# Optimization experiments

Hardware: AMD Instinct MI355X
Metric: run time of the kernel (lower is better)

Reference implementation:

```python
import jax, jax.numpy as jnp
import numpy as np
from jax import lax

N = 4096  # minibatch size / number of points


def _pairwise_dist(x):
    # x: (N, d) -> (N, N) euclidean distance matrix, symmetric, zero diagonal
    sq = jnp.sum(x * x, axis=-1)
    d2 = sq[:, None] + sq[None, :] - 2.0 * (x @ x.T)
    d2 = jnp.maximum(d2, 0.0)
    d = jnp.sqrt(d2)
    return d * (1.0 - jnp.eye(x.shape[0], dtype=x.dtype))


def setup_inputs() -> dict:
    key = jax.random.key(0)
    k1, k2 = jax.random.split(key)
    x_in = jax.random.normal(k1, (N, 32), dtype=jnp.float32)   # input-space points
    x_lat = jax.random.normal(k2, (N, 8), dtype=jnp.float32)   # latent-space points
    return {
        "input_distances": _pairwise_dist(x_in),
        "latent_distances": _pairwise_dist(x_lat),
    }


def _mst_edges(D):
    """Prim's algorithm on a dense distance matrix.

    Returns (N-1, 2) int32 edges (parent_in_tree, new_node). With distinct
    edge weights (random point clouds) the MST is unique, so this matches
    the original union-find/Kruskal get_mst_edges(one_root=True) edge set.
    """
    n = D.shape[0]
    in_tree0 = jnp.zeros((n,), dtype=bool).at[0].set(True)
    dist0 = D[0]                          # best distance from tree to each node
    parent0 = jnp.zeros((n,), dtype=jnp.int32)

    def step(carry, _):
        dist, parent, in_tree = carry
        masked = jnp.where(in_tree, jnp.inf, dist)
        j = jnp.argmin(masked).astype(jnp.int32)  # nearest non-tree node
        edge = jnp.stack([parent[j], j])
        in_tree = in_tree.at[j].set(True)
        row = D[j]                         # relax: distances via new node j
        better = row < dist
        dist = jnp.where(better, row, dist)
        parent = jnp.where(better, j, parent)
        return (dist, parent, in_tree), edge

    _, edges = lax.scan(step, (dist0, parent0, in_tree0), None, length=n - 1)
    return edges  # (N-1, 2)


def _select(D, pairs):
    return D[pairs[:, 0], pairs[:, 1]]


def reference(input_distances, latent_distances):
    pairs1 = _mst_edges(input_distances)
    pairs2 = _mst_edges(latent_distances)
    sig1 = _select(input_distances, pairs1)
    sig2 = _select(latent_distances, pairs2)
    sig1_2 = _select(latent_distances, pairs1)
    sig2_1 = _select(input_distances, pairs2)
    distance1_2 = jnp.sum((sig1 - sig1_2) ** 2)
    distance2_1 = jnp.sum((sig2 - sig2_1) ** 2)
    return distance1_2 + distance2_1
```

## Files before the change

### kernel.cpp

```cpp
#include <hip/hip_runtime.h>
#include <stdint.h>


#define NPTS 4096
#define NCHUNK 64
#define NBLK 1024
#define ROUNDS 12

typedef unsigned long long u64;

__device__ __forceinline__ u64 umin64(u64 a, u64 b) { return a < b ? a : b; }

__device__ __forceinline__ u64 pack_edge(float w, int i, int j) {
    unsigned wb = __float_as_uint(w);
    int u = i < j ? i : j;
    int v = i < j ? j : i;
    return ((u64)wb << 24) | ((u64)(unsigned)u << 12) | (u64)(unsigned)v;
}

__device__ __forceinline__ u64 wave_min64(u64 v) {
    #pragma unroll
    for (int off = 32; off; off >>= 1)
        v = umin64(v, __shfl_down(v, (unsigned)off, 64));
    return v;
}

__global__ __launch_bounds__(256) void tile_k(
    const float* __restrict__ D1, const float* __restrict__ D2,
    u64* __restrict__ cand) {
    int pb = blockIdx.x >> 12;
    int t  = blockIdx.x & 4095;
    int r = t >> 6, c = t & 63;
    if (r > c) return;
    const float* __restrict__ D = pb ? D2 : D1;
    u64* __restrict__ cnd = cand + (size_t)pb * NPTS * NCHUNK;

    __shared__ float ts[64][65];
    int R0 = r << 6, C0 = c << 6;
    int tid = threadIdx.x;

    #pragma unroll
    for (int e = 0; e < 4; ++e) {
        int idx4 = tid + e * 256;
        int row = idx4 >> 4, c4 = idx4 & 15;
        const float4* __restrict__ rp =
            (const float4*)(D + (size_t)(R0 + row) * NPTS + C0);
        float4 w = rp[c4];
        ts[row][c4 * 4    ] = w.x; ts[row][c4 * 4 + 1] = w.y;
        ts[row][c4 * 4 + 2] = w.z; ts[row][c4 * 4 + 3] = w.w;
    }
    __syncthreads();

    int wave = tid >> 6, lane = tid & 63;
    if (wave == 0) {
        int i = R0 + lane;
        float wm = 3.4e38f; int jm = 0;
        if (r == c) {
            for (int j = 0; j < 64; ++j) {
                float x = ts[lane][j];
                if ((C0 + j) != i && x < wm) { wm = x; jm = C0 + j; }
            }
        } else {
            for (int j = 0; j < 64; ++j) {
                float x = ts[lane][j];
                if (x < wm) { wm = x; jm = C0 + j; }
            }
        }
        cnd[i * NCHUNK + c] = pack_edge(wm, i, jm);
    } else if (wave == 1 && r != c) {
        int jcol = C0 + lane;
        float wm = 3.4e38f; int im = 0;
        for (int k2 = 0; k2 < 64; ++k2) {
            float x = ts[k2][lane];
            if (x < wm) { wm = x; im = R0 + k2; }
        }
        cnd[jcol * NCHUNK + r] = pack_edge(wm, jcol, im);
    }
}

__global__ __launch_bounds__(256) void finalize_k(
    u64* __restrict__ best, const u64* __restrict__ cand,
    int* __restrict__ done, float* __restrict__ out) {
    if (blockIdx.x == 0 && threadIdx.x == 0) {
        done[0] = 0; done[1] = 0; out[0] = 0.f;
    }
    int pb = blockIdx.x >> 10;
    int rb = blockIdx.x & (NBLK - 1);
    const u64* __restrict__ cnd = cand + (size_t)pb * NPTS * NCHUNK;
    int wave = threadIdx.x >> 6, lane = threadIdx.x & 63;
    int i = rb * 4 + wave;
    u64 bv = wave_min64(cnd[i * NCHUNK + lane]);
    if (lane == 0) best[pb * NPTS + i] = bv;
}

__global__ __launch_bounds__(256) void warm_k(
    const float* __restrict__ D1, const float* __restrict__ D2,
    u64* __restrict__ best, const int* __restrict__ comp,
    const int* __restrict__ done, u64* __restrict__ cand) {
    int pb = blockIdx.x >> 10;
    if (done[pb]) return;
    int rb = blockIdx.x & (NBLK - 1);
    const float* __restrict__ D = pb ? D2 : D1;
    const int* __restrict__ cmpg = comp + pb * NPTS;
    u64* __restrict__ bst = best + pb * NPTS;
    u64* __restrict__ cnd = cand + (size_t)pb * NPTS * NCHUNK;

    int wave = threadIdx.x >> 6, lane = threadIdx.x & 63;
    int i = rb * 4 + wave;
    int ci = cmpg[i];

    u64 live = ~0ull;
    bool dead = false;
    u64 c = cnd[i * NCHUNK + lane];
    if (c != ~0ull) {
        int u = (int)((c >> 12) & 0xFFF), v = (int)(c & 0xFFF);
        int j = (u == i) ? v : u;
        if (cmpg[j] != ci) live = c;
        else dead = true;
    }

    u64 extra = ~0ull;
    u64 mask = __ballot(dead);
    if (mask) {
        const float4* __restrict__ rowf = (const float4*)(D + (size_t)i * NPTS);
        const int4* __restrict__ cmp4 = (const int4*)cmpg;
        int g = lane >> 4, m16 = lane & 15;
        while (mask) {
            int kq = -1;
            #pragma unroll
            for (int s = 0; s < 4; ++s) {
                int kk = mask ? (int)(__ffsll((long long)mask) - 1) : -1;
                if (kk >= 0) mask &= mask - 1;
                if (s == g) kq = kk;
            }
            u64 e = ~0ull;
            if (kq >= 0) {
                float4 w = rowf[kq * 16 + m16];
                int4 cj = cmp4[kq * 16 + m16];
                int j0 = kq * 64 + m16 * 4;
                if (cj.x != ci) e = umin64(e, pack_edge(w.x, i, j0));
                if (cj.y != ci) e = umin64(e, pack_edge(w.y, i, j0 + 1));
                if (cj.z != ci) e = umin64(e, pack_edge(w.z, i, j0 + 2));
                if (cj.w != ci) e = umin64(e, pack_edge(w.w, i, j0 + 3));
            }
            #pragma unroll
            for (int off = 8; off; off >>= 1)
                e = umin64(e, __shfl_down(e, (unsigned)off, 16));
            if (kq >= 0 && m16 == 0) {
                cnd[i * NCHUNK + kq] = e;
                extra = umin64(extra, e);
            }
        }
    }
    u64 rmin = wave_min64(umin64(live, extra));
    if (lane == 0 && rmin != ~0ull && rmin < bst[ci]) atomicMin(&bst[ci], rmin);
}

__global__ __launch_bounds__(1024) void contract_k(
    const float* __restrict__ D1, const float* __restrict__ D2,
    u64* __restrict__ best, int* __restrict__ comp,
    int* __restrict__ done, float* __restrict__ out, int identity) {
    int pb = blockIdx.x;
    if (!identity && done[pb]) return;
    u64* __restrict__ bst = best + pb * NPTS;
    int* __restrict__ cmp = comp + pb * NPTS;

    __shared__ int link_s[NPTS];
    __shared__ float red_s[16];
    __shared__ int flag_s;
    int t = threadIdx.x;
    float loss = 0.f;

    int eu[4], ev[4], nl[4];
    bool act[4];

    for (int q = 0; q < 4; ++q) {
        int c = t + q * 1024;
        u64 b = bst[c];
        bool a = (b != ~0ull);
        act[q] = a;
        int u = (int)((b >> 12) & 0xFFF), v = (int)(b & 0xFFF);
        eu[q] = u; ev[q] = v;
        int l = c;
        if (a) {
            if (identity) l = (u == c) ? v : u;
            else { int cu = cmp[u]; l = (cu == c) ? cmp[v] : cu; }
        }
        link_s[c] = l;
    }
    __syncthreads();

    for (int q = 0; q < 4; ++q) {
        int c = t + q * 1024;
        int l = link_s[c];
        bool is2 = (l != c) && (link_s[l] == c);
        if (act[q] && !(is2 && c > l)) {
            size_t off = (size_t)eu[q] * NPTS + ev[q];
            float d = D1[off] - D2[off];
            loss += d * d;
        }
        nl[q] = (is2 && c < l) ? c : l;
    }
    __syncthreads();
    for (int q = 0; q < 4; ++q) link_s[t + q * 1024] = nl[q];
    __syncthreads();

    for (int it = 0; it < 13; ++it) {
        if (t == 0) flag_s = 0;
        __syncthreads();
        bool ch = false;
        for (int q = 0; q < 4; ++q) {
            int c = t + q * 1024;
            int l = link_s[c];
            int ll = link_s[l];
            nl[q] = ll;
            ch |= (ll != l);
        }
        if (ch) flag_s = 1;
        __syncthreads();
        for (int q = 0; q < 4; ++q) link_s[t + q * 1024] = nl[q];
        __syncthreads();
        if (!flag_s) break;
    }

    int c0 = identity ? 0 : cmp[0];
    __syncthreads();
    int root0 = link_s[c0];
    int same = 1;
    for (int q = 0; q < 4; ++q) {
        int v = t + q * 1024;
        int oc = identity ? v : cmp[v];
        int r = link_s[oc];
        cmp[v] = r;
        same &= (r == root0);
        bst[v] = ~0ull;
    }
    int all = __syncthreads_and(same);
    if (all && t == 0) done[pb] = 1;

    #pragma unroll
    for (int off = 32; off; off >>= 1) loss += __shfl_down(loss, (unsigned)off, 64);
    int wave = t >> 6, lane = t & 63;
    if (lane == 0) red_s[wave] = loss;
    __syncthreads();
    if (t == 0) {
        float s = 0.f;
        for (int wv = 0; wv < 16; ++wv) s += red_s[wv];
        atomicAdd(out, s);
    }
}

extern "C" void kernel_launch(void* const* d_in, const int* in_sizes, int n_in,
                              void* d_out, int out_size, void* d_ws, size_t ws_size,
                              hipStream_t stream) {
    const float* D1 = (const float*)d_in[0];
    const float* D2 = (const float*)d_in[1];
    float* out = (float*)d_out;

    char* ws = (char*)d_ws;
    u64* best = (u64*)ws;
    int* comp = (int*)(ws + 65536);
    int* done = (int*)(ws + 65536 + 32768);
    u64* cand = (u64*)(ws + 98312);

    tile_k<<<2 * 4096, 256, 0, stream>>>(D1, D2, cand);
    finalize_k<<<2 * NBLK, 256, 0, stream>>>(best, cand, done, out);
    contract_k<<<2, 1024, 0, stream>>>(D1, D2, best, comp, done, out, 1);
    for (int r = 1; r < ROUNDS; ++r) {
        warm_k<<<2 * NBLK, 256, 0, stream>>>(D1, D2, best, comp, done, cand);
        contract_k<<<2, 1024, 0, stream>>>(D1, D2, best, comp, done, out, 0);
    }
}
```

Baseline: 136.5 us.

## Fuse contraction into finalize and warm kernels via last-block-done counter

Removes the separate contract_k launches. Each finalize_k and warm_k block now increments a per-problem atomic counter, and the last block to arrive runs the component contraction and loss accumulation itself, as a 256-thread block. A small init kernel resets the counters, done flags and output. The aim is to cut about eleven kernel launches and their inter-kernel gaps from the Borůvka round loop. In exchange, each contraction runs on a quarter of the previous thread count, and correctness now relies on atomic ordering between blocks.

After: 442.4 us. +224.0%, slower.

```diff
diff --git a/kernel.cpp b/kernel.cpp
--- a/kernel.cpp
+++ b/kernel.cpp
@@ -23,6 +23,105 @@
     for (int off = 32; off; off >>= 1)
         v = umin64(v, __shfl_down(v, (unsigned)off, 64));
     return v;
+}
+
+__device__ void contract_block(
+    const float* __restrict__ D1, const float* __restrict__ D2,
+    u64* bst, int* cmp, int* done, float* out, int identity, int pb) {
+    __shared__ int link_s[NPTS];
+    __shared__ float red_s[4];
+    __shared__ int flag_s;
+    int t = threadIdx.x;
+    u64 b_[16];
+
+    #pragma unroll
+    for (int s = 0; s < 16; ++s) {
+        int c = t + s * 256;
+        u64 b = __hip_atomic_load(&bst[c], __ATOMIC_RELAXED,
+                                  __HIP_MEMORY_SCOPE_AGENT);
+        b_[s] = b;
+        int l = c;
+        if (b != ~0ull) {
+            int u = (int)((b >> 12) & 0xFFF), v = (int)(b & 0xFFF);
+            if (identity) l = (u == c) ? v : u;
+            else { int cu = cmp[u]; l = (cu == c) ? cmp[v] : cu; }
+        }
+        link_s[c] = l;
+    }
+    __syncthreads();
+
+    float loss = 0.f;
+    #pragma unroll
+    for (int s = 0; s < 16; ++s) {
+        int c = t + s * 256;
+        u64 b = b_[s];
+        int l = link_s[c];
+        bool is2 = (l != c) && (link_s[l] == c);
+        if (b != ~0ull && !(is2 && c > l)) {
+            int u = (int)((b >> 12) & 0xFFF), v = (int)(b & 0xFFF);
+            size_t off = (size_t)u * NPTS + v;
+            float d = D1[off] - D2[off];
+            loss += d * d;
+        }
+        b_[s] = (u64)(unsigned)((is2 && c < l) ? c : l);
+    }
+    __syncthreads();
+    #pragma unroll
+    for (int s = 0; s < 16; ++s) link_s[t + s * 256] = (int)b_[s];
+    __syncthreads();
+
+    for (int it = 0; it < 13; ++it) {
+        if (t == 0) flag_s = 0;
+        __syncthreads();
+        bool ch = false;
+        #pragma unroll
+        for (int s = 0; s < 16; ++s) {
+            int c = t + s * 256;
+            int l = link_s[c];
+            int ll = link_s[l];
+            b_[s] = (u64)(unsigned)ll;
+            ch |= (ll != l);
+        }
+        if (ch) flag_s = 1;
+        __syncthreads();
+        #pragma unroll
+        for (int s = 0; s < 16; ++s) link_s[t + s * 256] = (int)b_[s];
+        __syncthreads();
+        if (!flag_s) break;
+    }
+
+    int c0 = identity ? 0 : cmp[0];
+    __syncthreads();
+    int root0 = link_s[c0];
+    int same = 1;
+    #pragma unroll
+    for (int s = 0; s < 16; ++s) {
+        int v = t + s * 256;
+        int oc = identity ? v : cmp[v];
+        int r = link_s[oc];
+        cmp[v] = r;
+        same &= (r == root0);
+        bst[v] = ~0ull;
+    }
+    int all = __syncthreads_and(same);
+    if (all && t == 0) done[pb] = 1;
+
+    #pragma unroll
+    for (int off = 32; off; off >>= 1)
+        loss += __shfl_down(loss, (unsigned)off, 64);
+    int wv = t >> 6, lane = t & 63;
+    if (lane == 0) red_s[wv] = loss;
+    __syncthreads();
+    if (t == 0) atomicAdd(out, red_s[0] + red_s[1] + red_s[2] + red_s[3]);
+}
+
+__global__ __launch_bounds__(64) void init_k(
+    int* __restrict__ done, float* __restrict__ out, int* __restrict__ cnt) {
+    int t = threadIdx.x;
+    if (t < 32) cnt[t] = 0;
+    else if (t == 32) done[0] = 0;
+    else if (t == 33) done[1] = 0;
+    else if (t == 34) out[0] = 0.f;
 }
 
 __global__ __launch_bounds__(256) void tile_k(
@@ -79,30 +178,43 @@
 }
 
 __global__ __launch_bounds__(256) void finalize_k(
-    u64* __restrict__ best, const u64* __restrict__ cand,
-    int* __restrict__ done, float* __restrict__ out) {
-    if (blockIdx.x == 0 && threadIdx.x == 0) {
-        done[0] = 0; done[1] = 0; out[0] = 0.f;
-    }
+    const float* __restrict__ D1, const float* __restrict__ D2,
+    u64* best, const u64* __restrict__ cand, int* comp,
+    int* done, float* out, int* cnt) {
+    __shared__ int islast;
     int pb = blockIdx.x >> 10;
     int rb = blockIdx.x & (NBLK - 1);
     const u64* __restrict__ cnd = cand + (size_t)pb * NPTS * NCHUNK;
+    u64* bst = best + pb * NPTS;
+
     int wave = threadIdx.x >> 6, lane = threadIdx.x & 63;
     int i = rb * 4 + wave;
     u64 bv = wave_min64(cnd[i * NCHUNK + lane]);
-    if (lane == 0) best[pb * NPTS + i] = bv;
+    if (lane == 0)
+        __hip_atomic_store(&bst[i], bv, __ATOMIC_RELAXED,
+                           __HIP_MEMORY_SCOPE_AGENT);
+    __syncthreads();
+    if (threadIdx.x == 0) {
+        int old = __hip_atomic_fetch_add(&cnt[pb], 1, __ATOMIC_ACQ_REL,
+                                         __HIP_MEMORY_SCOPE_AGENT);
+        islast = (old == NBLK - 1);
+    }
+    __syncthreads();
+    if (islast)
+        contract_block(D1, D2, bst, comp + pb * NPTS, done, out, 1, pb);
 }
 
 __global__ __launch_bounds__(256) void warm_k(
     const float* __restrict__ D1, const float* __restrict__ D2,
-    u64* __restrict__ best, const int* __restrict__ comp,
-    const int* __restrict__ done, u64* __restrict__ cand) {
+    u64* best, int* comp, int* done, u64* __restrict__ cand,
+    float* out, int* cnt) {
+    __shared__ int islast;
     int pb = blockIdx.x >> 10;
     if (done[pb]) return;
     int rb = blockIdx.x & (NBLK - 1);
     const float* __restrict__ D = pb ? D2 : D1;
     const int* __restrict__ cmpg = comp + pb * NPTS;
-    u64* __restrict__ bst = best + pb * NPTS;
+    u64* bst = best + pb * NPTS;
     u64* __restrict__ cnd = cand + (size_t)pb * NPTS * NCHUNK;
 
     int wave = threadIdx.x >> 6, lane = threadIdx.x & 63;
@@ -154,100 +266,16 @@
     }
     u64 rmin = wave_min64(umin64(live, extra));
     if (lane == 0 && rmin != ~0ull && rmin < bst[ci]) atomicMin(&bst[ci], rmin);
-}
-
-__global__ __launch_bounds__(1024) void contract_k(
-    const float* __restrict__ D1, const float* __restrict__ D2,
-    u64* __restrict__ best, int* __restrict__ comp,
-    int* __restrict__ done, float* __restrict__ out, int identity) {
-    int pb = blockIdx.x;
-    if (!identity && done[pb]) return;
-    u64* __restrict__ bst = best + pb * NPTS;
-    int* __restrict__ cmp = comp + pb * NPTS;
-
-    __shared__ int link_s[NPTS];
-    __shared__ float red_s[16];
-    __shared__ int flag_s;
-    int t = threadIdx.x;
-    float loss = 0.f;
-
-    int eu[4], ev[4], nl[4];
-    bool act[4];
-
-    for (int q = 0; q < 4; ++q) {
-        int c = t + q * 1024;
-        u64 b = bst[c];
-        bool a = (b != ~0ull);
-        act[q] = a;
-        int u = (int)((b >> 12) & 0xFFF), v = (int)(b & 0xFFF);
-        eu[q] = u; ev[q] = v;
-        int l = c;
-        if (a) {
-            if (identity) l = (u == c) ? v : u;
-            else { int cu = cmp[u]; l = (cu == c) ? cmp[v] : cu; }
-        }
-        link_s[c] = l;
-    }
-    __syncthreads();
-
-    for (int q = 0; q < 4; ++q) {
-        int c = t + q * 1024;
-        int l = link_s[c];
-        bool is2 = (l != c) && (link_s[l] == c);
-        if (act[q] && !(is2 && c > l)) {
-            size_t off = (size_t)eu[q] * NPTS + ev[q];
-            float d = D1[off] - D2[off];
-            loss += d * d;
-        }
-        nl[q] = (is2 && c < l) ? c : l;
-    }
-    __syncthreads();
-    for (int q = 0; q < 4; ++q) link_s[t + q * 1024] = nl[q];
-    __syncthreads();
-
-    for (int it = 0; it < 13; ++it) {
-        if (t == 0) flag_s = 0;
-        __syncthreads();
-        bool ch = false;
-        for (int q = 0; q < 4; ++q) {
-            int c = t + q * 1024;
-            int l = link_s[c];
-            int ll = link_s[l];
-            nl[q] = ll;
-            ch |= (ll != l);
-        }
-        if (ch) flag_s = 1;
-        __syncthreads();
-        for (int q = 0; q < 4; ++q) link_s[t + q * 1024] = nl[q];
-        __syncthreads();
-        if (!flag_s) break;
-    }
-
-    int c0 = identity ? 0 : cmp[0];
-    __syncthreads();
-    int root0 = link_s[c0];
-    int same = 1;
-    for (int q = 0; q < 4; ++q) {
-        int v = t + q * 1024;
-        int oc = identity ? v : cmp[v];
-        int r = link_s[oc];
-        cmp[v] = r;
-        same &= (r == root0);
-        bst[v] = ~0ull;
-    }
-    int all = __syncthreads_and(same);
-    if (all && t == 0) done[pb] = 1;
-
-    #pragma unroll
-    for (int off = 32; off; off >>= 1) loss += __shfl_down(loss, (unsigned)off, 64);
-    int wave = t >> 6, lane = t & 63;
-    if (lane == 0) red_s[wave] = loss;
-    __syncthreads();
-    if (t == 0) {
-        float s = 0.f;
-        for (int wv = 0; wv < 16; ++wv) s += red_s[wv];
-        atomicAdd(out, s);
-    }
+
+    __syncthreads();
+    if (threadIdx.x == 0) {
+        int old = __hip_atomic_fetch_add(&cnt[pb], 1, __ATOMIC_ACQ_REL,
+                                         __HIP_MEMORY_SCOPE_AGENT);
+        islast = (old == NBLK - 1);
+    }
+    __syncthreads();
+    if (islast)
+        contract_block(D1, D2, bst, comp + pb * NPTS, done, out, 0, pb);
 }
 
 extern "C" void kernel_launch(void* const* d_in, const int* in_sizes, int n_in,
@@ -261,13 +289,15 @@
     u64* best = (u64*)ws;
     int* comp = (int*)(ws + 65536);
     int* done = (int*)(ws + 65536 + 32768);
-    u64* cand = (u64*)(ws + 98312);
-
+    int* cnt  = (int*)(ws + 98312);
+    u64* cand = (u64*)(ws + 98440);
+
+    init_k<<<1, 64, 0, stream>>>(done, out, cnt);
     tile_k<<<2 * 4096, 256, 0, stream>>>(D1, D2, cand);
-    finalize_k<<<2 * NBLK, 256, 0, stream>>>(best, cand, done, out);
-    contract_k<<<2, 1024, 0, stream>>>(D1, D2, best, comp, done, out, 1);
+    finalize_k<<<2 * NBLK, 256, 0, stream>>>(D1, D2, best, cand, comp,
+                                             done, out, cnt);
     for (int r = 1; r < ROUNDS; ++r) {
-        warm_k<<<2 * NBLK, 256, 0, stream>>>(D1, D2, best, comp, done, cand);
-        contract_k<<<2, 1024, 0, stream>>>(D1, D2, best, comp, done, out, 0);
-    }
-}
+        warm_k<<<2 * NBLK, 256, 0, stream>>>(D1, D2, best, comp, done, cand,
+                                             out, cnt + 2 * r);
+    }
+}
```
